# Kernel tuning notes

Measured on AMD Instinct MI355X. Metric: run time of the kernel, lower is better.

The kernel has to match this reference:

```python
import jax, jax.numpy as jnp
import numpy as np

B, S, HID = 2, 2048, 2048
NH, HD = 16, 128
EPS = 1e-5
ROPE_BASE = 10000.0


def setup_inputs() -> dict:
    key = jax.random.key(0)
    k1, k2, k3 = jax.random.split(key, 3)
    std = 1.0 / np.sqrt(HID)
    x = jax.random.normal(k1, (B, S, HID), jnp.float32)
    w_in = jax.random.truncated_normal(k2, -3.0, 3.0, (3 * NH * HD, HID), jnp.float32) * std
    std_o = std / np.sqrt(2.0)  # layer_id = 0 -> std / sqrt(2*(0+1))
    w_out = jax.random.truncated_normal(k3, -3.0, 3.0, (HID, NH * HD), jnp.float32) * std_o
    q_norm_w = jnp.ones((NH * HD,), jnp.float32)
    k_norm_w = jnp.ones((NH * HD,), jnp.float32)
    return {"x": x, "w_in": w_in, "w_out": w_out, "q_norm_w": q_norm_w, "k_norm_w": k_norm_w}


def _rms_norm(x, w, eps=EPS):
    ms = jnp.mean(x * x, axis=-1, keepdims=True)
    return x * jax.lax.rsqrt(ms + eps) * w


def _rope(x, offset=0):
    # x: [B, S, NH, HD]; rotate-half convention
    half = HD // 2
    inv_freq = 1.0 / (ROPE_BASE ** (jnp.arange(half, dtype=jnp.float32) / half))
    pos = jnp.arange(x.shape[1], dtype=jnp.float32) + offset
    ang = pos[:, None] * inv_freq                      # [S, half]
    cos = jnp.cos(ang)[None, :, None, :]
    sin = jnp.sin(ang)[None, :, None, :]
    x1, x2 = jnp.split(x, 2, axis=-1)
    return jnp.concatenate([x1 * cos - x2 * sin, x2 * cos + x1 * sin], axis=-1)


def reference(x, w_in, w_out, q_norm_w, k_norm_w):
    b, s, _ = x.shape
    qkv = jnp.einsum('bsh,oh->bso', x, w_in)           # [B, S, 3*NH*HD]
    q, k, v = jnp.split(qkv, 3, axis=-1)
    # qk-norm over the flat (NH*HD) axis, as in the torch module
    q = _rms_norm(q, q_norm_w)
    k = _rms_norm(k, k_norm_w)
    q = q.reshape(b, s, NH, HD)
    k = k.reshape(b, s, NH, HD)
    v = v.reshape(b, s, NH, HD)
    q = _rope(q)
    k = _rope(k)
    scale = 1.0 / np.sqrt(HD)
    scores = jnp.einsum('bqhd,bkhd->bhqk', q, k) * scale
    causal = jnp.tril(jnp.ones((s, s), dtype=bool))
    scores = jnp.where(causal[None, None, :, :], scores, jnp.finfo(scores.dtype).min)
    probs = jax.nn.softmax(scores, axis=-1)
    out = jnp.einsum('bhqk,bkhd->bqhd', probs, v).reshape(b, s, NH * HD)
    return jnp.einsum('bso,ho->bsh', out, w_out)
```

## Files before the change

kernel.cpp:

```cpp
#include <hip/hip_runtime.h>
#include <hip/hip_bf16.h>
#include <math.h>

#define B_   2
#define S_   2048
#define HID_ 2048
#define NH_  16
#define HD_  128
#define QKV_ (3 * NH_ * HD_)
#define EPS_ 1e-5f

typedef __bf16 bf16x8 __attribute__((ext_vector_type(8)));
typedef __bf16 bf16x4 __attribute__((ext_vector_type(4)));
typedef __bf16 bf16x2 __attribute__((ext_vector_type(2)));
typedef float  f32x4  __attribute__((ext_vector_type(4)));

__global__ __launch_bounds__(256) void cast3_f32_bf16(
    const float* __restrict__ a, __bf16* __restrict__ ao, int na4,
    const float* __restrict__ b, __bf16* __restrict__ bo, int nb4,
    const float* __restrict__ c, __bf16* __restrict__ co, int nc4) {
    int j = blockIdx.x * 256 + threadIdx.x;
    const float* src;
    __bf16* dst;
    if (j < na4) {
        src = a; dst = ao;
    } else {
        j -= na4;
        if (j < nb4) {
            src = b; dst = bo;
        } else {
            j -= nb4;
            if (j >= nc4) return;
            src = c; dst = co;
        }
    }
    float4 v = reinterpret_cast<const float4*>(src)[j];
    bf16x4 o = {(__bf16)v.x, (__bf16)v.y, (__bf16)v.z, (__bf16)v.w};
    reinterpret_cast<bf16x4*>(dst)[j] = o;
}

__device__ __forceinline__ void gload_lds16(const __bf16* g, __bf16* l) {
    __builtin_amdgcn_global_load_lds(
        (const __attribute__((address_space(1))) void*)g,
        (__attribute__((address_space(3))) void*)l, 16, 0, 0);
}

__device__ __forceinline__ void stage_tile6(
    const __bf16* pA, const __bf16* pB, __bf16* buf, int w, int K) {
#pragma unroll
    for (int s = 0; s < 2; ++s)
        gload_lds16(pA + (size_t)s * 64 * K, buf + s * 4096 + w * 512);
#pragma unroll
    for (int s = 0; s < 4; ++s)
        gload_lds16(pB + (size_t)s * 64 * K, buf + 8192 + s * 4096 + w * 512);
}

template <typename OutT>
__global__ __launch_bounds__(512, 2) void gemm_bt_8ph(
    const __bf16* __restrict__ A, const __bf16* __restrict__ Bm,
    OutT* __restrict__ C, int M, int N, int K) {
    __shared__ __bf16 lds[3][24576];

    const int tid  = threadIdx.x;
    const int w    = tid >> 6;
    const int lane = tid & 63;
    const int lrow = lane & 15;
    const int quad = lane >> 4;
    const int wm   = w >> 2;
    const int wn   = w & 3;

    const int chunk = (int)gridDim.x >> 3;
    const int flat  = (int)blockIdx.x;
    const int vid   = (flat & 7) * chunk + (flat >> 3);
    const int by    = vid & 31;
    const int bx    = vid >> 5;
    const int m0 = by * 128;
    const int n0 = bx * 256;

    const int lr = lane >> 3;
    const int lg = lane & 7;
    const __bf16* pA = A  + (size_t)(m0 + w * 8 + lr) * K + ((lg ^ lr) << 3);
    const __bf16* pB = Bm + (size_t)(n0 + w * 8 + lr) * K + ((lg ^ lr) << 3);

    const int nt = K >> 6;
    f32x4 acc[4][4] = {};

    stage_tile6(pA, pB, &lds[0][0], w, K);
    stage_tile6(pA + 64, pB + 64, &lds[1][0], w, K);

    int cur = 0;
    for (int t = 0; t < nt; ++t) {
        __bf16* bufc = &lds[cur][0];
        int nxt = cur + 2; if (nxt >= 3) nxt -= 3;
        if (t + 2 < nt) {
            stage_tile6(pA + (size_t)(t + 2) * 64, pB + (size_t)(t + 2) * 64,
                        &lds[nxt][0], w, K);
            asm volatile("s_waitcnt vmcnt(12)" ::: "memory");
        } else if (t + 1 < nt) {
            asm volatile("s_waitcnt vmcnt(6)" ::: "memory");
        } else {
            asm volatile("s_waitcnt vmcnt(0)" ::: "memory");
        }
        __builtin_amdgcn_s_barrier();
        asm volatile("" ::: "memory");

#pragma unroll
        for (int q = 0; q < 2; ++q) {
            bf16x8 af[2][2], bfv[4][2];
#pragma unroll
            for (int i = 0; i < 2; ++i)
#pragma unroll
                for (int kk = 0; kk < 2; ++kk)
                    af[i][kk] = *reinterpret_cast<const bf16x8*>(
                        &bufc[(wm * 64 + (q * 2 + i) * 16 + lrow) * 64 +
                              (((kk * 4 + quad) ^ (lrow & 7)) << 3)]);
#pragma unroll
            for (int j = 0; j < 4; ++j)
#pragma unroll
                for (int kk = 0; kk < 2; ++kk)
                    bfv[j][kk] = *reinterpret_cast<const bf16x8*>(
                        &bufc[8192 + (wn * 64 + j * 16 + lrow) * 64 +
                              (((kk * 4 + quad) ^ (lrow & 7)) << 3)]);
            __builtin_amdgcn_s_barrier();
            asm volatile("" ::: "memory");
            __builtin_amdgcn_s_setprio(1);
#pragma unroll
            for (int i = 0; i < 2; ++i)
#pragma unroll
                for (int j = 0; j < 4; ++j)
#pragma unroll
                    for (int kk = 0; kk < 2; ++kk)
                        acc[q * 2 + i][j] =
                            __builtin_amdgcn_mfma_f32_16x16x32_bf16(
                                af[i][kk], bfv[j][kk], acc[q * 2 + i][j],
                                0, 0, 0);
            __builtin_amdgcn_s_setprio(0);
        }
        __builtin_amdgcn_s_barrier();
        asm volatile("" ::: "memory");
        cur = (cur == 2) ? 0 : cur + 1;
    }

#pragma unroll
    for (int mi = 0; mi < 4; ++mi) {
#pragma unroll
        for (int r = 0; r < 4; ++r) {
            int row = m0 + wm * 64 + mi * 16 + quad * 4 + r;
            size_t basec = (size_t)row * N + n0 + wn * 64 + lrow;
#pragma unroll
            for (int nj = 0; nj < 4; ++nj)
                C[basec + nj * 16] = (OutT)acc[mi][nj][r];
        }
    }
}

__global__ __launch_bounds__(256) void normrope_kernel(
    __bf16* __restrict__ qkv, const float* __restrict__ qw,
    const float* __restrict__ kw) {
    const int row = blockIdx.x;
    const int sel = blockIdx.y;
    const int pos = row & (S_ - 1);
    __bf16* p = qkv + (size_t)row * QKV_ + sel * 2048;
    const float* w = sel ? kw : qw;

    __shared__ float buf[2048];
    __shared__ float red[4];
    const int tid = threadIdx.x;
    const int e   = tid * 8;

    bf16x8 t = *reinterpret_cast<const bf16x8*>(&p[e]);
    float xs[8];
    float ss = 0.f;
#pragma unroll
    for (int u = 0; u < 8; ++u) {
        xs[u] = (float)t[u];
        buf[e + u] = xs[u];
        ss += xs[u] * xs[u];
    }
#pragma unroll
    for (int off = 32; off > 0; off >>= 1) ss += __shfl_xor(ss, off, 64);
    if ((tid & 63) == 0) red[tid >> 6] = ss;
    __syncthreads();
    float total = red[0] + red[1] + red[2] + red[3];
    float scale = rsqrtf(total * (1.f / 2048.f) + EPS_);

    const float kfreq2 = -0.20762050593046f;
    const int jbase = e & 63;
    const bool first = (e & 127) < 64;
    const int ep = e ^ 64;

    float ps[8], ws[8], pw[8];
#pragma unroll
    for (int u = 0; u < 8; ++u) ps[u] = buf[ep + u];
    float4 w0 = *reinterpret_cast<const float4*>(&w[e]);
    float4 w1 = *reinterpret_cast<const float4*>(&w[e + 4]);
    float4 p0 = *reinterpret_cast<const float4*>(&w[ep]);
    float4 p1 = *reinterpret_cast<const float4*>(&w[ep + 4]);
    ws[0]=w0.x; ws[1]=w0.y; ws[2]=w0.z; ws[3]=w0.w;
    ws[4]=w1.x; ws[5]=w1.y; ws[6]=w1.z; ws[7]=w1.w;
    pw[0]=p0.x; pw[1]=p0.y; pw[2]=p0.z; pw[3]=p0.w;
    pw[4]=p1.x; pw[5]=p1.y; pw[6]=p1.z; pw[7]=p1.w;

    bf16x8 o8;
#pragma unroll
    for (int u = 0; u < 8; ++u) {
        float inv_freq = exp2f((float)(jbase + u) * kfreq2);
        float ang = (float)pos * inv_freq;
        float sn = __sinf(ang);
        float cs = __cosf(ang);
        float a  = xs[u] * scale * ws[u];
        float bb = ps[u] * scale * pw[u];
        float o  = first ? (a * cs - bb * sn) : (a * cs + bb * sn);
        o8[u] = (__bf16)o;
    }
    *reinterpret_cast<bf16x8*>(&p[e]) = o8;
}

#define VTP 36

__global__ __launch_bounds__(512, 4) void attn_mfma(
    const __bf16* __restrict__ qkv, __bf16* __restrict__ aout) {
    const int flat = (int)blockIdx.x;
    const int vid  = (flat & 7) * 64 + (flat >> 3);
    const int bh   = vid >> 4;
    const int qt   = 15 - (vid & 15);
    const int b    = bh >> 4;
    const int h    = bh & (NH_ - 1);
    const int q0   = qt * 128;
    const int tid  = threadIdx.x;
    const int w    = tid >> 6;
    const int lane = tid & 63;
    const int lrow = lane & 15;
    const int quad = lane >> 4;

    __shared__ __bf16 Ks[2][4][32 * 32];
    __shared__ __bf16 Vt[2][128 * VTP];
    __shared__ __bf16 Pb[8][16 * VTP];

    const size_t base = (size_t)(b * S_) * QKV_ + (size_t)h * HD_;
    const int qrow = q0 + w * 16 + lrow;

    bf16x8 qf[4];
#pragma unroll
    for (int kc = 0; kc < 4; ++kc)
        qf[kc] = *reinterpret_cast<const bf16x8*>(
            &qkv[base + (size_t)qrow * QKV_ + kc * 32 + quad * 8]);

    f32x4 o[8] = {};
    float lpart = 0.f;

    const int ktmax_w   = 4 * qt + (w >> 1);
    const int ktmax_blk = 4 * qt + 3;
    const float sl2 = 0.12751743671f;

    const __bf16* kg0 = qkv + base + 2048 +
                        (size_t)((w & 1) * 16 + (lane >> 2)) * QKV_ +
                        (w >> 1) * 32 + (lane & 3) * 8;
    const int g  = tid >> 4;
    const int kp = tid & 15;
    const __bf16* vg0 = qkv + base + 4096 + (size_t)(kp * 2) * QKV_ + g * 8;

    gload_lds16(kg0, &Ks[0][w >> 1][(w & 1) * 512]);
    bf16x8 v0 = {}, v1 = {};
    if (tid < 256) {
        v0 = *reinterpret_cast<const bf16x8*>(vg0);
        v1 = *reinterpret_cast<const bf16x8*>(vg0 + QKV_);
    }

    for (int kt = 0; kt <= ktmax_blk; ++kt) {
        const int buf = kt & 1;
        if (tid < 256) {
#pragma unroll
            for (int u = 0; u < 8; ++u) {
                bf16x2 pr = {v0[u], v1[u]};
                *reinterpret_cast<bf16x2*>(
                    &Vt[buf][(g * 8 + u) * VTP + kp * 2]) = pr;
            }
        }
        __syncthreads();
        if (kt < ktmax_blk) {
            const __bf16* kg = kg0 + (size_t)(kt + 1) * 32 * QKV_;
            gload_lds16(kg, &Ks[buf ^ 1][w >> 1][(w & 1) * 512]);
            if (tid < 256) {
                const __bf16* vg = vg0 + (size_t)(kt + 1) * 32 * QKV_;
                v0 = *reinterpret_cast<const bf16x8*>(vg);
                v1 = *reinterpret_cast<const bf16x8*>(vg + QKV_);
            }
        }
        if (kt <= ktmax_w) {
            f32x4 sc[2] = {};
            __builtin_amdgcn_s_setprio(1);
#pragma unroll
            for (int kc = 0; kc < 4; ++kc) {
                bf16x8 kf0 = *reinterpret_cast<const bf16x8*>(
                    &Ks[buf][kc][lrow * 32 + quad * 8]);
                bf16x8 kf1 = *reinterpret_cast<const bf16x8*>(
                    &Ks[buf][kc][(16 + lrow) * 32 + quad * 8]);
                sc[0] = __builtin_amdgcn_mfma_f32_16x16x32_bf16(
                    kf0, qf[kc], sc[0], 0, 0, 0);
                sc[1] = __builtin_amdgcn_mfma_f32_16x16x32_bf16(
                    kf1, qf[kc], sc[1], 0, 0, 0);
            }
            __builtin_amdgcn_s_setprio(0);
            const bool diag = (kt == ktmax_w);
            float p[2][4];
#pragma unroll
            for (int m2 = 0; m2 < 2; ++m2)
#pragma unroll
                for (int r = 0; r < 4; ++r) {
                    float s = sc[m2][r] * sl2 - 32.f;
                    if (diag && kt * 32 + m2 * 16 + quad * 4 + r > qrow)
                        s = -1e30f;
                    p[m2][r] = exp2f(s);
                    lpart += p[m2][r];
                }
#pragma unroll
            for (int m2 = 0; m2 < 2; ++m2) {
                bf16x4 pb = {(__bf16)p[m2][0], (__bf16)p[m2][1],
                             (__bf16)p[m2][2], (__bf16)p[m2][3]};
                *reinterpret_cast<bf16x4*>(
                    &Pb[w][lrow * VTP + m2 * 16 + quad * 4]) = pb;
            }
            bf16x8 pf = *reinterpret_cast<const bf16x8*>(
                &Pb[w][lrow * VTP + quad * 8]);
            __builtin_amdgcn_s_setprio(1);
#pragma unroll
            for (int dt = 0; dt < 8; ++dt) {
                bf16x8 vf = *reinterpret_cast<const bf16x8*>(
                    &Vt[buf][(dt * 16 + lrow) * VTP + quad * 8]);
                o[dt] = __builtin_amdgcn_mfma_f32_16x16x32_bf16(
                    vf, pf, o[dt], 0, 0, 0);
            }
            __builtin_amdgcn_s_setprio(0);
        }
    }

    lpart += __shfl_xor(lpart, 16, 64);
    lpart += __shfl_xor(lpart, 32, 64);
    const float invl = 1.f / lpart;
    const size_t orow = (size_t)(b * S_ + qrow) * (NH_ * HD_) + (size_t)h * HD_;
#pragma unroll
    for (int dt = 0; dt < 8; ++dt) {
        bf16x4 ov = {(__bf16)(o[dt][0] * invl), (__bf16)(o[dt][1] * invl),
                     (__bf16)(o[dt][2] * invl), (__bf16)(o[dt][3] * invl)};
        *reinterpret_cast<bf16x4*>(&aout[orow + dt * 16 + quad * 4]) = ov;
    }
}

extern "C" void kernel_launch(void* const* d_in, const int* in_sizes, int n_in,
                              void* d_out, int out_size, void* d_ws,
                              size_t ws_size, hipStream_t stream) {
    const float* x     = (const float*)d_in[0];
    const float* w_in  = (const float*)d_in[1];
    const float* w_out = (const float*)d_in[2];
    const float* qw    = (const float*)d_in[3];
    const float* kw    = (const float*)d_in[4];
    float* out = (float*)d_out;

    const int M = B_ * S_;
    char* ws = (char*)d_ws;
    __bf16* qkv_b   = (__bf16*)(ws);
    __bf16* w_out_b = (__bf16*)(ws + (size_t)50331648);
    __bf16* x_b     = (__bf16*)(ws + (size_t)58720256);
    __bf16* attn_b  = x_b;
    __bf16* w_in_b  = (__bf16*)(ws + (size_t)75497472);

    dim3 blk(256);

    {
        const int na4 = (M * HID_) / 4;
        const int nb4 = (QKV_ * HID_) / 4;
        const int nc4 = (HID_ * NH_ * HD_) / 4;
        const int tot = na4 + nb4 + nc4;
        cast3_f32_bf16<<<dim3((tot + 255) / 256), blk, 0, stream>>>(
            x, x_b, na4, w_in, w_in_b, nb4, w_out, w_out_b, nc4);
    }

    gemm_bt_8ph<__bf16><<<dim3((M / 128) * (QKV_ / 256)), dim3(512), 0,
                          stream>>>(x_b, w_in_b, qkv_b, M, QKV_, HID_);
    normrope_kernel<<<dim3(M, 2), blk, 0, stream>>>(qkv_b, qw, kw);
    attn_mfma<<<dim3((S_ / 128) * B_ * NH_), dim3(512), 0, stream>>>(
        qkv_b, attn_b);
    gemm_bt_8ph<float><<<dim3((M / 128) * (HID_ / 256)), dim3(512), 0,
                         stream>>>(attn_b, w_out_b, out, M, HID_, NH_ * HD_);
}
```

Measured before the change: 417.0 us.

## Enlarge GEMM tiles to 256x256 with double-buffered interleaved staging

Replaces the 128x256-tile, triple-buffered GEMM with a 256x256-tile, double-buffered kernel. Each K step is split into four phases that interleave LDS reads, MFMA groups and async global-to-LDS loads of the next tile, so each warp now holds 8x4 accumulators. The larger tile raises data reuse and cuts global traffic per flop, at the cost of fewer blocks (occupancy and tail balance at M=4096), more registers, and more barriers per step.

```diff
diff --git a/kernel.cpp b/kernel.cpp
--- a/kernel.cpp
+++ b/kernel.cpp
@@ -45,21 +45,54 @@
         (__attribute__((address_space(3))) void*)l, 16, 0, 0);
 }
 
-__device__ __forceinline__ void stage_tile6(
-    const __bf16* pA, const __bf16* pB, __bf16* buf, int w, int K) {
-#pragma unroll
-    for (int s = 0; s < 2; ++s)
-        gload_lds16(pA + (size_t)s * 64 * K, buf + s * 4096 + w * 512);
-#pragma unroll
-    for (int s = 0; s < 4; ++s)
-        gload_lds16(pB + (size_t)s * 64 * K, buf + 8192 + s * 4096 + w * 512);
+#define BARR  __builtin_amdgcn_s_barrier()
+#define LGKM0 asm volatile("s_waitcnt lgkmcnt(0)" ::: "memory")
+#define FENCE asm volatile("" ::: "memory")
+
+__device__ __forceinline__ void read_a4(const __bf16* bc, int wm, int lrow,
+                                        int quad, int swz, int qq,
+                                        bf16x8 (&af)[2][2]) {
+#pragma unroll
+    for (int i2 = 0; i2 < 2; ++i2)
+#pragma unroll
+        for (int kk = 0; kk < 2; ++kk)
+            af[i2][kk] = *reinterpret_cast<const bf16x8*>(
+                &bc[(wm * 128 + (qq * 2 + i2) * 16 + lrow) * 64 +
+                    (((kk * 4 + quad) ^ swz) << 3)]);
+}
+
+__device__ __forceinline__ void read_b8(const __bf16* bc, int wn, int lrow,
+                                        int quad, int swz,
+                                        bf16x8 (&bf)[4][2]) {
+#pragma unroll
+    for (int j = 0; j < 4; ++j)
+#pragma unroll
+        for (int kk = 0; kk < 2; ++kk)
+            bf[j][kk] = *reinterpret_cast<const bf16x8*>(
+                &bc[16384 + (wn * 64 + j * 16 + lrow) * 64 +
+                    (((kk * 4 + quad) ^ swz) << 3)]);
+}
+
+__device__ __forceinline__ void mfma16(int qq, const bf16x8 (&af)[2][2],
+                                       const bf16x8 (&bf)[4][2],
+                                       f32x4 (&acc)[8][4]) {
+    __builtin_amdgcn_s_setprio(1);
+#pragma unroll
+    for (int i2 = 0; i2 < 2; ++i2)
+#pragma unroll
+        for (int j = 0; j < 4; ++j)
+#pragma unroll
+            for (int kk = 0; kk < 2; ++kk)
+                acc[qq * 2 + i2][j] = __builtin_amdgcn_mfma_f32_16x16x32_bf16(
+                    af[i2][kk], bf[j][kk], acc[qq * 2 + i2][j], 0, 0, 0);
+    __builtin_amdgcn_s_setprio(0);
 }
 
 template <typename OutT>
-__global__ __launch_bounds__(512, 2) void gemm_bt_8ph(
+__global__ __launch_bounds__(512, 2) void gemm_bt_256(
     const __bf16* __restrict__ A, const __bf16* __restrict__ Bm,
     OutT* __restrict__ C, int M, int N, int K) {
-    __shared__ __bf16 lds[3][24576];
+    __shared__ __bf16 lds[2][32768];
 
     const int tid  = threadIdx.x;
     const int w    = tid >> 6;
@@ -68,88 +101,100 @@
     const int quad = lane >> 4;
     const int wm   = w >> 2;
     const int wn   = w & 3;
+    const int swz  = lrow & 7;
 
     const int chunk = (int)gridDim.x >> 3;
     const int flat  = (int)blockIdx.x;
     const int vid   = (flat & 7) * chunk + (flat >> 3);
-    const int by    = vid & 31;
-    const int bx    = vid >> 5;
-    const int m0 = by * 128;
-    const int n0 = bx * 256;
+    const int m0 = (vid & 15) * 256;
+    const int n0 = (vid >> 4) * 256;
 
     const int lr = lane >> 3;
     const int lg = lane & 7;
+    const size_t K64 = (size_t)K * 64;
     const __bf16* pA = A  + (size_t)(m0 + w * 8 + lr) * K + ((lg ^ lr) << 3);
     const __bf16* pB = Bm + (size_t)(n0 + w * 8 + lr) * K + ((lg ^ lr) << 3);
 
+#define STA(c, tt, dst) gload_lds16(pA + (size_t)(c) * K64 + (size_t)(tt) * 64, \
+                                    (dst) + (c) * 4096 + w * 512)
+#define STB(c, tt, dst) gload_lds16(pB + (size_t)(c) * K64 + (size_t)(tt) * 64, \
+                                    (dst) + 16384 + (c) * 4096 + w * 512)
+
+    f32x4 acc[8][4] = {};
+    bf16x8 af[2][2], bf[4][2];
+
+    {
+        __bf16* d = &lds[0][0];
+        STB(0, 0, d); STB(1, 0, d); STB(2, 0, d); STB(3, 0, d);
+        FENCE;
+        STA(0, 0, d); STA(2, 0, d);
+        FENCE;
+        STA(1, 0, d); STA(3, 0, d);
+    }
+    asm volatile("s_waitcnt vmcnt(2)" ::: "memory");
+    BARR;
+
     const int nt = K >> 6;
-    f32x4 acc[4][4] = {};
-
-    stage_tile6(pA, pB, &lds[0][0], w, K);
-    stage_tile6(pA + 64, pB + 64, &lds[1][0], w, K);
-
-    int cur = 0;
-    for (int t = 0; t < nt; ++t) {
-        __bf16* bufc = &lds[cur][0];
-        int nxt = cur + 2; if (nxt >= 3) nxt -= 3;
-        if (t + 2 < nt) {
-            stage_tile6(pA + (size_t)(t + 2) * 64, pB + (size_t)(t + 2) * 64,
-                        &lds[nxt][0], w, K);
-            asm volatile("s_waitcnt vmcnt(12)" ::: "memory");
-        } else if (t + 1 < nt) {
-            asm volatile("s_waitcnt vmcnt(6)" ::: "memory");
-        } else {
-            asm volatile("s_waitcnt vmcnt(0)" ::: "memory");
-        }
-        __builtin_amdgcn_s_barrier();
-        asm volatile("" ::: "memory");
-
-#pragma unroll
-        for (int q = 0; q < 2; ++q) {
-            bf16x8 af[2][2], bfv[4][2];
-#pragma unroll
-            for (int i = 0; i < 2; ++i)
-#pragma unroll
-                for (int kk = 0; kk < 2; ++kk)
-                    af[i][kk] = *reinterpret_cast<const bf16x8*>(
-                        &bufc[(wm * 64 + (q * 2 + i) * 16 + lrow) * 64 +
-                              (((kk * 4 + quad) ^ (lrow & 7)) << 3)]);
+    for (int t = 0; t < nt - 1; ++t) {
+        __bf16* bc = &lds[t & 1][0];
+        __bf16* bn = &lds[(t & 1) ^ 1][0];
+        const int tn = t + 1;
+        read_a4(bc, wm, lrow, quad, swz, 0, af);
+        read_b8(bc, wn, lrow, quad, swz, bf);
+        STB(0, tn, bn); STB(1, tn, bn);
+        BARR; LGKM0;
+        mfma16(0, af, bf, acc);
+        BARR;
+        read_a4(bc, wm, lrow, quad, swz, 1, af);
+        STB(2, tn, bn); STB(3, tn, bn);
+        BARR; LGKM0;
+        mfma16(1, af, bf, acc);
+        asm volatile("s_waitcnt vmcnt(4)" ::: "memory");
+        BARR;
+        read_a4(bc, wm, lrow, quad, swz, 2, af);
+        STA(0, tn, bn); STA(2, tn, bn);
+        BARR; LGKM0;
+        mfma16(2, af, bf, acc);
+        BARR;
+        read_a4(bc, wm, lrow, quad, swz, 3, af);
+        STA(1, tn, bn); STA(3, tn, bn);
+        BARR; LGKM0;
+        mfma16(3, af, bf, acc);
+        asm volatile("s_waitcnt vmcnt(2)" ::: "memory");
+        BARR;
+    }
+    {
+        __bf16* bc = &lds[(nt - 1) & 1][0];
+        read_a4(bc, wm, lrow, quad, swz, 0, af);
+        read_b8(bc, wn, lrow, quad, swz, bf);
+        BARR; LGKM0;
+        mfma16(0, af, bf, acc);
+        BARR;
+        read_a4(bc, wm, lrow, quad, swz, 1, af);
+        BARR; LGKM0;
+        mfma16(1, af, bf, acc);
+        asm volatile("s_waitcnt vmcnt(0)" ::: "memory");
+        BARR;
+        read_a4(bc, wm, lrow, quad, swz, 2, af);
+        BARR; LGKM0;
+        mfma16(2, af, bf, acc);
+        BARR;
+        read_a4(bc, wm, lrow, quad, swz, 3, af);
+        BARR; LGKM0;
+        mfma16(3, af, bf, acc);
+    }
+#undef STA
+#undef STB
+
+#pragma unroll
+    for (int mf = 0; mf < 8; ++mf) {
+#pragma unroll
+        for (int r = 0; r < 4; ++r) {
+            int row = m0 + wm * 128 + mf * 16 + quad * 4 + r;
+            size_t cb = (size_t)row * N + n0 + wn * 64 + lrow;
 #pragma unroll
             for (int j = 0; j < 4; ++j)
-#pragma unroll
-                for (int kk = 0; kk < 2; ++kk)
-                    bfv[j][kk] = *reinterpret_cast<const bf16x8*>(
-                        &bufc[8192 + (wn * 64 + j * 16 + lrow) * 64 +
-                              (((kk * 4 + quad) ^ (lrow & 7)) << 3)]);
-            __builtin_amdgcn_s_barrier();
-            asm volatile("" ::: "memory");
-            __builtin_amdgcn_s_setprio(1);
-#pragma unroll
-            for (int i = 0; i < 2; ++i)
-#pragma unroll
-                for (int j = 0; j < 4; ++j)
-#pragma unroll
-                    for (int kk = 0; kk < 2; ++kk)
-                        acc[q * 2 + i][j] =
-                            __builtin_amdgcn_mfma_f32_16x16x32_bf16(
-                                af[i][kk], bfv[j][kk], acc[q * 2 + i][j],
-                                0, 0, 0);
-            __builtin_amdgcn_s_setprio(0);
-        }
-        __builtin_amdgcn_s_barrier();
-        asm volatile("" ::: "memory");
-        cur = (cur == 2) ? 0 : cur + 1;
-    }
-
-#pragma unroll
-    for (int mi = 0; mi < 4; ++mi) {
-#pragma unroll
-        for (int r = 0; r < 4; ++r) {
-            int row = m0 + wm * 64 + mi * 16 + quad * 4 + r;
-            size_t basec = (size_t)row * N + n0 + wn * 64 + lrow;
-#pragma unroll
-            for (int nj = 0; nj < 4; ++nj)
-                C[basec + nj * 16] = (OutT)acc[mi][nj][r];
+                C[cb + j * 16] = (OutT)acc[mf][j][r];
         }
     }
 }
@@ -376,11 +421,11 @@
             x, x_b, na4, w_in, w_in_b, nb4, w_out, w_out_b, nc4);
     }
 
-    gemm_bt_8ph<__bf16><<<dim3((M / 128) * (QKV_ / 256)), dim3(512), 0,
+    gemm_bt_256<__bf16><<<dim3((M / 256) * (QKV_ / 256)), dim3(512), 0,
                           stream>>>(x_b, w_in_b, qkv_b, M, QKV_, HID_);
     normrope_kernel<<<dim3(M, 2), blk, 0, stream>>>(qkv_b, qw, kw);
     attn_mfma<<<dim3((S_ / 128) * B_ * NH_), dim3(512), 0, stream>>>(
         qkv_b, attn_b);
-    gemm_bt_8ph<float><<<dim3((M / 128) * (HID_ / 256)), dim3(512), 0,
+    gemm_bt_256<float><<<dim3((M / 256) * (HID_ / 256)), dim3(512), 0,
                          stream>>>(attn_b, w_out_b, out, M, HID_, NH_ * HD_);
 }
```

Result: no change. 418.7 us (+0.4%).
